# Performance work log

Hardware: AMD Instinct MI355X
Metric: run time of the kernel (lower is better)

Reference implementation:

```python
import jax, jax.numpy as jnp
import numpy as np

ROPE_BASE = 10000.0

def _rms_norm(x):
    eps = jnp.asarray(jnp.finfo(x.dtype).eps, x.dtype)
    return x * jax.lax.rsqrt(jnp.mean(x * x, axis=-1, keepdims=True) + eps)

def _rope(x):
    # x: [B, S, H, hd]; rotate-halves variant: y1 = x1*cos + x2*sin, y2 = -x1*sin + x2*cos
    S, hd = x.shape[1], x.shape[3]
    d = hd // 2
    inv_freq = 1.0 / (ROPE_BASE ** (jnp.arange(0, hd, 2, dtype=jnp.float32) / hd))  # [d]
    t = jnp.arange(S, dtype=jnp.float32)
    freqs = jnp.outer(t, inv_freq)                       # [S, d]
    cos = jnp.cos(freqs)[None, :, None, :].astype(x.dtype)
    sin = jnp.sin(freqs)[None, :, None, :].astype(x.dtype)
    x1, x2 = x[..., :d], x[..., d:]
    return jnp.concatenate([x1 * cos + x2 * sin, -x1 * sin + x2 * cos], axis=-1)

def setup_inputs() -> dict:
    key = jax.random.key(0)
    ks = jax.random.split(key, 7)
    B, S, D = 1, 2048, 1024
    std = 0.02
    return {
        "x": jax.random.normal(ks[0], (B, S, D), jnp.float32),
        "v1": jax.random.normal(ks[1], (B, S, D), jnp.float32),
        "Wq": jax.random.normal(ks[2], (D, D), jnp.float32) * std,
        "Wk": jax.random.normal(ks[3], (D, D), jnp.float32) * std,
        "Wv": jax.random.normal(ks[4], (D, D), jnp.float32) * std,
        "Wout": jax.random.normal(ks[5], (D, D), jnp.float32) * std,
        "lambdas": jnp.float32(0.5),
        "n_heads": 16,
    }

def reference(x, v1, Wq, Wk, Wv, Wout, lambdas, n_heads):
    B, S, D = x.shape
    H = n_heads
    hd = D // H
    # QKV projections (CastedLinear, no bias)
    q = (x @ Wq.T).reshape(B, S, H, hd)
    k = (x @ Wk.T).reshape(B, S, H, hd)
    v = (x @ Wv.T).reshape(B, S, H, hd)
    # value residual mix with first-layer values v1
    v = (1.0 - lambdas) * v + lambdas * v1.reshape(B, S, H, hd)
    # per-head RMS norm (no learned scale) then RoPE
    q, k = _rms_norm(q), _rms_norm(k)
    q, k = _rope(q), _rope(k)
    # causal attention (flex_attention default: softmax, scale 1/sqrt(hd))
    scale = 1.0 / jnp.sqrt(jnp.asarray(hd, x.dtype))
    scores = jnp.einsum('bqhd,bkhd->bhqk', q, k) * scale        # [B,H,S,S]
    causal = jnp.tril(jnp.ones((S, S), dtype=bool))
    scores = jnp.where(causal[None, None], scores, jnp.asarray(-jnp.inf, scores.dtype))
    p = jax.nn.softmax(scores, axis=-1)
    y = jnp.einsum('bhqk,bkhd->bqhd', p, v).reshape(B, S, D)
    y = y @ Wout.T
    return (y, v1)
```

## Files before the change

kernel.cpp:

```cpp
#include <hip/hip_runtime.h>
#include <hip/hip_bf16.h>

#define S_LEN 2048
#define D_DIM 1024
#define NH    16
#define NEG_BIG (-1.0e30f)

#define EPI_NORMROPE   1
#define EPI_VMIX_T     2
#define EPI_F32        3
#define EPI_NORMROPE_Q 4
#define EPI_F32A       5

typedef __attribute__((ext_vector_type(8))) short bf16x8;
typedef __attribute__((ext_vector_type(4))) float f32x4;
typedef const __attribute__((address_space(1))) unsigned char gu8_t;
typedef __attribute__((address_space(3))) unsigned char lu8_t;

__device__ __forceinline__ float bf2f(unsigned short h) {
    union { unsigned int u; float f; } v; v.u = ((unsigned int)h) << 16; return v.f;
}
__device__ __forceinline__ unsigned short f2b(float f) {
    union { float f; unsigned int u; } v; v.f = f;
    unsigned int u = v.u;
    return (unsigned short)((u + 0x7FFFu + ((u >> 16) & 1u)) >> 16);
}
__device__ __forceinline__ unsigned short f2b_trunc(float f) {
    union { float f; unsigned int u; } v; v.f = f;
    return (unsigned short)(v.u >> 16);
}

__global__ __launch_bounds__(256)
void to_bf16(const float* __restrict__ x,  const float* __restrict__ wq,
             const float* __restrict__ wk, const float* __restrict__ wv,
             const float* __restrict__ wo, const float* __restrict__ v1,
             unsigned short* __restrict__ xb,  unsigned short* __restrict__ wqb,
             unsigned short* __restrict__ wkb, unsigned short* __restrict__ wvb,
             unsigned short* __restrict__ wob, float* __restrict__ v1dst)
{
    const int z = blockIdx.y;
    int i8 = blockIdx.x * 256 + threadIdx.x;
    if (z == 5) {
        const float* sp = v1 + (size_t)i8 * 8;
        float4 lo = *(const float4*)sp, hi = *(const float4*)(sp + 4);
        float* dp = v1dst + (size_t)i8 * 8;
        *(float4*)dp = lo; *(float4*)(dp + 4) = hi;
        return;
    }
    const float* s; unsigned short* d; int n;
    switch (z) {
        case 0: s = x;  d = xb;  n = S_LEN * D_DIM; break;
        case 1: s = wq; d = wqb; n = D_DIM * D_DIM; break;
        case 2: s = wk; d = wkb; n = D_DIM * D_DIM; break;
        case 3: s = wv; d = wvb; n = D_DIM * D_DIM; break;
        default: s = wo; d = wob; n = D_DIM * D_DIM; break;
    }
    if (i8 * 8 >= n) return;
    const float* sp = s + (size_t)i8 * 8;
    float4 lo = *(const float4*)sp, hi = *(const float4*)(sp + 4);
    uint4 p;
    p.x = f2b(lo.x) | ((unsigned)f2b(lo.y) << 16);
    p.y = f2b(lo.z) | ((unsigned)f2b(lo.w) << 16);
    p.z = f2b(hi.x) | ((unsigned)f2b(hi.y) << 16);
    p.w = f2b(hi.z) | ((unsigned)f2b(hi.w) << 16);
    *(uint4*)(d + (size_t)i8 * 8) = p;
}

__global__ __launch_bounds__(256, 3)
void gemm64(const unsigned short* __restrict__ A,
            const unsigned short* __restrict__ B0, const unsigned short* __restrict__ B1,
            const unsigned short* __restrict__ B2,
            void* __restrict__ C0, void* __restrict__ C1, void* __restrict__ C2,
            const float* __restrict__ vmix, const float* __restrict__ lam,
            int epiPack)
{
    const int which = blockIdx.z;
    const unsigned short* Bp = (which == 0) ? B0 : ((which == 1) ? B1 : B2);
    void* C = (which == 0) ? C0 : ((which == 1) ? C1 : C2);
    const int epi = (epiPack >> (8 * which)) & 0xff;
    const int tn = blockIdx.x * 128;
    const int tm = blockIdx.y * 64;

    __shared__ unsigned short Asl[64 * 32];
    __shared__ unsigned short Bsl[128 * 32];

    const int t    = threadIdx.x;
    const int lane = t & 63;
    const int wave = t >> 6;
    const int wm   = (wave >> 1) * 32;
    const int wn   = (wave & 1) * 64;
    const int lrow = lane & 15;
    const int quad = lane >> 4;
    const int srow = t >> 2;
    const int scol = (t & 3) * 8;

    f32x4 acc[2][4];
    #pragma unroll
    for (int i = 0; i < 2; ++i)
        #pragma unroll
        for (int j = 0; j < 4; ++j) {
            f32x4 z = {0.f, 0.f, 0.f, 0.f};
            acc[i][j] = z;
        }

    for (int k0 = 0; k0 < D_DIM; k0 += 32) {
        __builtin_amdgcn_global_load_lds(
            (gu8_t*)(A + (size_t)(tm + srow) * D_DIM + k0 + scol),
            (lu8_t*)&Asl[t * 8], 16, 0, 0);
        __builtin_amdgcn_global_load_lds(
            (gu8_t*)(Bp + (size_t)(tn + srow) * D_DIM + k0 + scol),
            (lu8_t*)&Bsl[t * 8], 16, 0, 0);
        __builtin_amdgcn_global_load_lds(
            (gu8_t*)(Bp + (size_t)(tn + 64 + srow) * D_DIM + k0 + scol),
            (lu8_t*)&Bsl[2048 + t * 8], 16, 0, 0);
        __syncthreads();
        bf16x8 af[2], bfr[4];
        #pragma unroll
        for (int i = 0; i < 2; ++i)
            af[i] = *(const bf16x8*)(&Asl[(wm + i * 16 + lrow) * 32 + quad * 8]);
        #pragma unroll
        for (int j = 0; j < 4; ++j)
            bfr[j] = *(const bf16x8*)(&Bsl[(wn + j * 16 + lrow) * 32 + quad * 8]);
        #pragma unroll
        for (int i = 0; i < 2; ++i)
            #pragma unroll
            for (int j = 0; j < 4; ++j)
                acc[i][j] = __builtin_amdgcn_mfma_f32_16x16x32_bf16(af[i], bfr[j], acc[i][j], 0, 0, 0);
        __syncthreads();
    }

    if (epi == EPI_NORMROPE || epi == EPI_NORMROPE_Q) {
        const float post = (epi == EPI_NORMROPE_Q) ? 0.18033688011112042f : 1.0f;
        #pragma unroll
        for (int i = 0; i < 2; ++i) {
            #pragma unroll
            for (int r = 0; r < 4; ++r) {
                int row = tm + wm + i * 16 + quad * 4 + r;
                float v0 = acc[i][0][r], v1 = acc[i][1][r];
                float v2 = acc[i][2][r], v3 = acc[i][3][r];
                float ss = v0 * v0 + v1 * v1 + v2 * v2 + v3 * v3;
                ss += __shfl_xor(ss, 1); ss += __shfl_xor(ss, 2);
                ss += __shfl_xor(ss, 4); ss += __shfl_xor(ss, 8);
                float rms = rsqrtf(ss * (1.f / 64.f) + 1.1920929e-7f) * post;
                v0 *= rms; v1 *= rms; v2 *= rms; v3 *= rms;
                float fs = (float)row;
                float a0 = fs * exp2f(-0.41524101186092030f * (float)lrow);
                float a1 = fs * exp2f(-0.41524101186092030f * (float)(16 + lrow));
                float s0, c0, s1, c1;
                __sincosf(a0, &s0, &c0);
                __sincosf(a1, &s1, &c1);
                unsigned short* Cb = (unsigned short*)C;
                size_t base = (size_t)row * D_DIM + tn + wn + lrow;
                Cb[base]      = f2b(v0 * c0 + v2 * s0);
                Cb[base + 16] = f2b(v1 * c1 + v3 * s1);
                Cb[base + 32] = f2b(-v0 * s0 + v2 * c0);
                Cb[base + 48] = f2b(-v1 * s1 + v3 * c1);
            }
        }
    } else if (epi == EPI_VMIX_T) {
        float lamf = *lam;
        #pragma unroll
        for (int i = 0; i < 2; ++i) {
            int cm0 = tm + wm + i * 16 + quad * 4;
            #pragma unroll
            for (int j = 0; j < 4; ++j) {
                int cn = tn + wn + j * 16 + lrow;
                ushort4 pk;
                float vals[4];
                #pragma unroll
                for (int r = 0; r < 4; ++r) {
                    size_t idx = (size_t)(cm0 + r) * D_DIM + cn;
                    vals[r] = (1.f - lamf) * acc[i][j][r] + lamf * vmix[idx];
                }
                pk.x = f2b(vals[0]); pk.y = f2b(vals[1]);
                pk.z = f2b(vals[2]); pk.w = f2b(vals[3]);
                *(ushort4*)((unsigned short*)C + (size_t)cn * S_LEN + cm0) = pk;
            }
        }
    } else {
        #pragma unroll
        for (int i = 0; i < 2; ++i) {
            int cm0 = tm + wm + i * 16 + quad * 4;
            #pragma unroll
            for (int j = 0; j < 4; ++j) {
                int cn = tn + wn + j * 16 + lrow;
                #pragma unroll
                for (int r = 0; r < 4; ++r)
                    ((float*)C)[(size_t)(cm0 + r) * D_DIM + cn] = acc[i][j][r];
            }
        }
    }
}

__global__ __launch_bounds__(256, 3)
void gemm_bt(const unsigned short* __restrict__ A,
             const unsigned short* __restrict__ B0,
             void* __restrict__ C0,
             const float* __restrict__ lam,
             int epi, int splitK)
{
    const int which = blockIdx.z;
    const unsigned short* Bp = B0;
    void* C = C0;
    int kLo = 0, kHi = D_DIM;
    if (splitK) { kLo = which * (D_DIM / 2); kHi = kLo + D_DIM / 2; }
    const int tn = blockIdx.x * 128;
    const int tm = blockIdx.y * 128;

    __shared__ unsigned short Asl[128 * 32];
    __shared__ unsigned short Bsl[128 * 32];

    const int t    = threadIdx.x;
    const int lane = t & 63;
    const int wave = t >> 6;
    const int wm   = (wave >> 1) * 64;
    const int wn   = (wave & 1) * 64;
    const int lrow = lane & 15;
    const int quad = lane >> 4;
    const int srow = lane >> 2;
    const int scol = (lane & 3) * 8;

    f32x4 acc[4][4];
    #pragma unroll
    for (int i = 0; i < 4; ++i)
        #pragma unroll
        for (int j = 0; j < 4; ++j) {
            f32x4 z = {0.f, 0.f, 0.f, 0.f};
            acc[i][j] = z;
        }

    for (int k0 = kLo; k0 < kHi; k0 += 32) {
        #pragma unroll
        for (int rep = 0; rep < 2; ++rep) {
            int grp = wave * 2 + rep;
            int row = grp * 16 + srow;
            __builtin_amdgcn_global_load_lds(
                (gu8_t*)(A + (size_t)(tm + row) * D_DIM + k0 + scol),
                (lu8_t*)&Asl[grp * 512], 16, 0, 0);
            __builtin_amdgcn_global_load_lds(
                (gu8_t*)(Bp + (size_t)(tn + row) * D_DIM + k0 + scol),
                (lu8_t*)&Bsl[grp * 512], 16, 0, 0);
        }
        __syncthreads();
        bf16x8 af[4], bfr[4];
        #pragma unroll
        for (int i = 0; i < 4; ++i)
            af[i] = *(const bf16x8*)(&Asl[(wm + i * 16 + lrow) * 32 + quad * 8]);
        #pragma unroll
        for (int j = 0; j < 4; ++j)
            bfr[j] = *(const bf16x8*)(&Bsl[(wn + j * 16 + lrow) * 32 + quad * 8]);
        #pragma unroll
        for (int i = 0; i < 4; ++i)
            #pragma unroll
            for (int j = 0; j < 4; ++j)
                acc[i][j] = __builtin_amdgcn_mfma_f32_16x16x32_bf16(af[i], bfr[j], acc[i][j], 0, 0, 0);
        __syncthreads();
    }

    if (epi == EPI_F32A) {
        #pragma unroll
        for (int i = 0; i < 4; ++i) {
            int cm0 = tm + wm + i * 16 + quad * 4;
            #pragma unroll
            for (int j = 0; j < 4; ++j) {
                int cn = tn + wn + j * 16 + lrow;
                #pragma unroll
                for (int r = 0; r < 4; ++r)
                    atomicAdd(&((float*)C)[(size_t)(cm0 + r) * D_DIM + cn], acc[i][j][r]);
            }
        }
    } else {
        #pragma unroll
        for (int i = 0; i < 4; ++i) {
            int cm0 = tm + wm + i * 16 + quad * 4;
            #pragma unroll
            for (int j = 0; j < 4; ++j) {
                int cn = tn + wn + j * 16 + lrow;
                #pragma unroll
                for (int r = 0; r < 4; ++r)
                    ((float*)C)[(size_t)(cm0 + r) * D_DIM + cn] = acc[i][j][r];
            }
        }
    }
}

__global__ __launch_bounds__(256, 4)
void attn_mfma(const unsigned short* Qb,
               const unsigned short* __restrict__ Kb,
               const unsigned short* __restrict__ Vtg,
               float* __restrict__ Opart, float* __restrict__ Lpart)
{
    const int bx = blockIdx.x;
    int qt, c;
    if (bx < 32)      { qt = 31 - (bx >> 2);            c = bx & 3;  }
    else if (bx < 56) { int i = bx - 32; qt = 23 - i/3; c = i % 3;   }
    else if (bx < 72) { int i = bx - 56; qt = 15 - (i>>1); c = i & 1;}
    else              { qt = 7 - (bx - 72);             c = 0;       }
    const int jlo = c * 8;
    const int jhi = min(jlo + 7, qt);
    const int h  = blockIdx.y;
    const int t  = threadIdx.x;
    const int w  = t >> 6;
    const int l  = t & 63;
    const int l15  = l & 15;
    const int quad = l >> 4;
    const int hco  = h * 64;
    const int slot = (qt * 4 + c) * NH + h;

    __shared__ unsigned short Ks[2][64][72];
    __shared__ unsigned short Vt[2][64][72];

    const unsigned short* qrow = Qb + (size_t)(qt * 64 + w * 16 + l15) * D_DIM + hco;
    bf16x8 qf0 = *(const bf16x8*)(qrow + quad * 8);
    bf16x8 qf1 = *(const bf16x8*)(qrow + 32 + quad * 8);

    f32x4 oac[4];
    #pragma unroll
    for (int nt = 0; nt < 4; ++nt) { f32x4 z = {0.f,0.f,0.f,0.f}; oac[nt] = z; }
    float lsum = 0.f;

    const int rr = t >> 2;
    const int dc = (t & 3) * 16;

    const unsigned short* kbase = Kb  + (size_t)rr * D_DIM + hco + dc;
    const unsigned short* vbase = Vtg + (size_t)(hco + rr) * S_LEN + dc;

    uint4 ka0, ka1, va0, va1;
    {
        const unsigned short* kp = kbase + (size_t)jlo * 64 * D_DIM;
        const unsigned short* vp = vbase + (size_t)jlo * 64;
        ka0 = *(const uint4*)kp;  ka1 = *(const uint4*)(kp + 8);
        va0 = *(const uint4*)vp;  va1 = *(const uint4*)(vp + 8);
    }

    const int q_g = qt * 64 + w * 16 + l15;
    const float C2 = -11.541560327111707f;

    for (int j = jlo; j <= jhi; ++j) {
        const int buf = (j - jlo) & 1;
        *(uint4*)&Ks[buf][rr][dc]     = ka0;
        *(uint4*)&Ks[buf][rr][dc + 8] = ka1;
        *(uint4*)&Vt[buf][rr][dc]     = va0;
        *(uint4*)&Vt[buf][rr][dc + 8] = va1;
        __syncthreads();
        if (j < jhi) {
            const unsigned short* kp = kbase + (size_t)(j + 1) * 64 * D_DIM;
            const unsigned short* vp = vbase + (size_t)(j + 1) * 64;
            ka0 = *(const uint4*)kp;  ka1 = *(const uint4*)(kp + 8);
            va0 = *(const uint4*)vp;  va1 = *(const uint4*)(vp + 8);
        }

        f32x4 sac[4];
        __builtin_amdgcn_s_setprio(1);
        #pragma unroll
        for (int nt = 0; nt < 4; ++nt) {
            f32x4 z = {0.f,0.f,0.f,0.f};
            bf16x8 kf0 = *(const bf16x8*)&Ks[buf][nt * 16 + l15][quad * 8];
            z = __builtin_amdgcn_mfma_f32_16x16x32_bf16(kf0, qf0, z, 0, 0, 0);
            bf16x8 kf1 = *(const bf16x8*)&Ks[buf][nt * 16 + l15][32 + quad * 8];
            z = __builtin_amdgcn_mfma_f32_16x16x32_bf16(kf1, qf1, z, 0, 0, 0);
            sac[nt] = z;
        }
        __builtin_amdgcn_s_setprio(0);

        unsigned short (*Psw)[72] = (unsigned short (*)[72])&Ks[buf ^ 1][w * 16];

        if (j < qt) {
            #pragma unroll
            for (int nt = 0; nt < 4; ++nt) {
                float pe0 = exp2f(sac[nt][0] + C2);
                float pe1 = exp2f(sac[nt][1] + C2);
                float pe2 = exp2f(sac[nt][2] + C2);
                float pe3 = exp2f(sac[nt][3] + C2);
                lsum += (pe0 + pe1) + (pe2 + pe3);
                ushort4 pk;
                pk.x = f2b_trunc(pe0); pk.y = f2b_trunc(pe1);
                pk.z = f2b_trunc(pe2); pk.w = f2b_trunc(pe3);
                *(ushort4*)&Psw[l15][nt * 16 + quad * 4] = pk;
            }
        } else {
            #pragma unroll
            for (int nt = 0; nt < 4; ++nt) {
                int key0 = j * 64 + nt * 16 + quad * 4;
                float pe[4];
                #pragma unroll
                for (int r = 0; r < 4; ++r) {
                    float s = sac[nt][r] + C2;
                    if (key0 + r > q_g) s = NEG_BIG;
                    pe[r] = exp2f(s);
                    lsum += pe[r];
                }
                ushort4 pk;
                pk.x = f2b_trunc(pe[0]); pk.y = f2b_trunc(pe[1]);
                pk.z = f2b_trunc(pe[2]); pk.w = f2b_trunc(pe[3]);
                *(ushort4*)&Psw[l15][nt * 16 + quad * 4] = pk;
            }
        }

        bf16x8 pf0 = *(const bf16x8*)&Psw[l15][quad * 8];
        bf16x8 pf1 = *(const bf16x8*)&Psw[l15][32 + quad * 8];
        __builtin_amdgcn_s_setprio(1);
        #pragma unroll
        for (int nt = 0; nt < 4; ++nt) {
            bf16x8 vf0 = *(const bf16x8*)&Vt[buf][nt * 16 + l15][quad * 8];
            oac[nt] = __builtin_amdgcn_mfma_f32_16x16x32_bf16(pf0, vf0, oac[nt], 0, 0, 0);
            bf16x8 vf1 = *(const bf16x8*)&Vt[buf][nt * 16 + l15][32 + quad * 8];
            oac[nt] = __builtin_amdgcn_mfma_f32_16x16x32_bf16(pf1, vf1, oac[nt], 0, 0, 0);
        }
        __builtin_amdgcn_s_setprio(0);
        __syncthreads();
    }

    float lr = lsum;
    lr += __shfl_xor(lr, 16);
    lr += __shfl_xor(lr, 32);
    if (l < 16)
        Lpart[(size_t)slot * 64 + w * 16 + l15] = lr;
    float* Op = Opart + (size_t)slot * 4096;
    #pragma unroll
    for (int nt = 0; nt < 4; ++nt)
        #pragma unroll
        for (int r = 0; r < 4; ++r)
            Op[(size_t)(w * 16 + quad * 4 + r) * 64 + nt * 16 + l15] = oac[nt][r];
}

__global__ __launch_bounds__(256)
void attn_combine(const float* __restrict__ Opart, const float* __restrict__ Lpart,
                  unsigned short* __restrict__ Ob, float* __restrict__ yzero)
{
    const int qt  = blockIdx.x;
    const int h   = blockIdx.y;
    const int t   = threadIdx.x;
    const int row = t >> 2;
    const int c0  = (t & 3) * 16;
    float acc[16];
    #pragma unroll
    for (int i = 0; i < 16; ++i) acc[i] = 0.f;
    float lsum = 0.f;
    for (int c = 0; c < 4; ++c) {
        if (c * 8 > qt) break;
        const size_t slot = (size_t)((qt * 4 + c) * NH + h);
        const float* Op = Opart + slot * 4096 + (size_t)row * 64 + c0;
        #pragma unroll
        for (int g = 0; g < 4; ++g) {
            float4 a = *(const float4*)(Op + g * 4);
            acc[g * 4 + 0] += a.x; acc[g * 4 + 1] += a.y;
            acc[g * 4 + 2] += a.z; acc[g * 4 + 3] += a.w;
        }
        lsum += Lpart[slot * 64 + row];
    }
    const float inv = 1.f / lsum;
    unsigned int pk[8];
    #pragma unroll
    for (int i = 0; i < 8; ++i)
        pk[i] = f2b(acc[2 * i] * inv) | ((unsigned)f2b(acc[2 * i + 1] * inv) << 16);
    unsigned short* dst = Ob + (size_t)(qt * 64 + row) * D_DIM + h * 64 + c0;
    *(uint4*)dst       = make_uint4(pk[0], pk[1], pk[2], pk[3]);
    *(uint4*)(dst + 8) = make_uint4(pk[4], pk[5], pk[6], pk[7]);

    const int flat = (h * 32 + qt) * 256 + t;
    float4 z4 = {0.f, 0.f, 0.f, 0.f};
    float4* yz = (float4*)(yzero + (size_t)flat * 16);
    yz[0] = z4; yz[1] = z4; yz[2] = z4; yz[3] = z4;
}

extern "C" void kernel_launch(void* const* d_in, const int* in_sizes, int n_in,
                              void* d_out, int out_size, void* d_ws, size_t ws_size,
                              hipStream_t stream)
{
    const float* x    = (const float*)d_in[0];
    const float* v1   = (const float*)d_in[1];
    const float* Wq   = (const float*)d_in[2];
    const float* Wk   = (const float*)d_in[3];
    const float* Wv   = (const float*)d_in[4];
    const float* Wout = (const float*)d_in[5];
    const float* lam  = (const float*)d_in[6];
    float* out = (float*)d_out;

    const size_t SD = (size_t)S_LEN * D_DIM;
    const size_t DD = (size_t)D_DIM * D_DIM;
    unsigned short* Qb  = (unsigned short*)d_ws;
    unsigned short* Kb  = Qb + SD;
    unsigned short* Vtg = Kb + SD;
    unsigned short* Ab  = Qb;
    float* Opart = (float*)(Vtg + SD);
    float* Lpart = Opart + (size_t)2048 * 4096;
    unsigned short* xb    = (unsigned short*)((char*)d_ws + (46u << 20));
    unsigned short* Woutb = (unsigned short*)((char*)d_ws + (50u << 20));

    unsigned short* Wqb   = (unsigned short*)d_out;
    unsigned short* Wkb   = Wqb + DD;
    unsigned short* Wvb   = Wkb + DD;

    to_bf16<<<dim3(1024, 6), 256, 0, stream>>>(
        x, Wq, Wk, Wv, Wout, v1, xb, Wqb, Wkb, Wvb, Woutb, out + SD);

    gemm64<<<dim3(D_DIM / 128, S_LEN / 64, 3), 256, 0, stream>>>(
        xb, Wqb, Wkb, Wvb, Qb, Kb, Vtg, v1, lam,
        EPI_NORMROPE_Q | (EPI_NORMROPE << 8) | (EPI_VMIX_T << 16));

    attn_mfma<<<dim3(80, NH), 256, 0, stream>>>(Qb, Kb, Vtg, Opart, Lpart);
    attn_combine<<<dim3(S_LEN / 64, NH), 256, 0, stream>>>(Opart, Lpart, Ab, out);

    gemm_bt<<<dim3(D_DIM / 128, S_LEN / 128, 2), 256, 0, stream>>>(
        Ab, Woutb, d_out, lam, EPI_F32A, 1);
}
```

Measured before the change: 173.4 us.

## Use 128-row query tiles in attention and replace split-K output GEMM

```diff
diff --git a/kernel.cpp b/kernel.cpp
--- a/kernel.cpp
+++ b/kernel.cpp
@@ -10,7 +10,6 @@
 #define EPI_VMIX_T     2
 #define EPI_F32        3
 #define EPI_NORMROPE_Q 4
-#define EPI_F32A       5
 
 typedef __attribute__((ext_vector_type(8))) short bf16x8;
 typedef __attribute__((ext_vector_type(4))) float f32x4;
@@ -192,98 +191,6 @@
     }
 }
 
-__global__ __launch_bounds__(256, 3)
-void gemm_bt(const unsigned short* __restrict__ A,
-             const unsigned short* __restrict__ B0,
-             void* __restrict__ C0,
-             const float* __restrict__ lam,
-             int epi, int splitK)
-{
-    const int which = blockIdx.z;
-    const unsigned short* Bp = B0;
-    void* C = C0;
-    int kLo = 0, kHi = D_DIM;
-    if (splitK) { kLo = which * (D_DIM / 2); kHi = kLo + D_DIM / 2; }
-    const int tn = blockIdx.x * 128;
-    const int tm = blockIdx.y * 128;
-
-    __shared__ unsigned short Asl[128 * 32];
-    __shared__ unsigned short Bsl[128 * 32];
-
-    const int t    = threadIdx.x;
-    const int lane = t & 63;
-    const int wave = t >> 6;
-    const int wm   = (wave >> 1) * 64;
-    const int wn   = (wave & 1) * 64;
-    const int lrow = lane & 15;
-    const int quad = lane >> 4;
-    const int srow = lane >> 2;
-    const int scol = (lane & 3) * 8;
-
-    f32x4 acc[4][4];
-    #pragma unroll
-    for (int i = 0; i < 4; ++i)
-        #pragma unroll
-        for (int j = 0; j < 4; ++j) {
-            f32x4 z = {0.f, 0.f, 0.f, 0.f};
-            acc[i][j] = z;
-        }
-
-    for (int k0 = kLo; k0 < kHi; k0 += 32) {
-        #pragma unroll
-        for (int rep = 0; rep < 2; ++rep) {
-            int grp = wave * 2 + rep;
-            int row = grp * 16 + srow;
-            __builtin_amdgcn_global_load_lds(
-                (gu8_t*)(A + (size_t)(tm + row) * D_DIM + k0 + scol),
-                (lu8_t*)&Asl[grp * 512], 16, 0, 0);
-            __builtin_amdgcn_global_load_lds(
-                (gu8_t*)(Bp + (size_t)(tn + row) * D_DIM + k0 + scol),
-                (lu8_t*)&Bsl[grp * 512], 16, 0, 0);
-        }
-        __syncthreads();
-        bf16x8 af[4], bfr[4];
-        #pragma unroll
-        for (int i = 0; i < 4; ++i)
-            af[i] = *(const bf16x8*)(&Asl[(wm + i * 16 + lrow) * 32 + quad * 8]);
-        #pragma unroll
-        for (int j = 0; j < 4; ++j)
-            bfr[j] = *(const bf16x8*)(&Bsl[(wn + j * 16 + lrow) * 32 + quad * 8]);
-        #pragma unroll
-        for (int i = 0; i < 4; ++i)
-            #pragma unroll
-            for (int j = 0; j < 4; ++j)
-                acc[i][j] = __builtin_amdgcn_mfma_f32_16x16x32_bf16(af[i], bfr[j], acc[i][j], 0, 0, 0);
-        __syncthreads();
-    }
-
-    if (epi == EPI_F32A) {
-        #pragma unroll
-        for (int i = 0; i < 4; ++i) {
-            int cm0 = tm + wm + i * 16 + quad * 4;
-            #pragma unroll
-            for (int j = 0; j < 4; ++j) {
-                int cn = tn + wn + j * 16 + lrow;
-                #pragma unroll
-                for (int r = 0; r < 4; ++r)
-                    atomicAdd(&((float*)C)[(size_t)(cm0 + r) * D_DIM + cn], acc[i][j][r]);
-            }
-        }
-    } else {
-        #pragma unroll
-        for (int i = 0; i < 4; ++i) {
-            int cm0 = tm + wm + i * 16 + quad * 4;
-            #pragma unroll
-            for (int j = 0; j < 4; ++j) {
-                int cn = tn + wn + j * 16 + lrow;
-                #pragma unroll
-                for (int r = 0; r < 4; ++r)
-                    ((float*)C)[(size_t)(cm0 + r) * D_DIM + cn] = acc[i][j][r];
-            }
-        }
-    }
-}
-
 __global__ __launch_bounds__(256, 4)
 void attn_mfma(const unsigned short* Qb,
                const unsigned short* __restrict__ Kb,
@@ -291,13 +198,19 @@
                float* __restrict__ Opart, float* __restrict__ Lpart)
 {
     const int bx = blockIdx.x;
-    int qt, c;
-    if (bx < 32)      { qt = 31 - (bx >> 2);            c = bx & 3;  }
-    else if (bx < 56) { int i = bx - 32; qt = 23 - i/3; c = i % 3;   }
-    else if (bx < 72) { int i = bx - 56; qt = 15 - (i>>1); c = i & 1;}
-    else              { qt = 7 - (bx - 72);             c = 0;       }
-    const int jlo = c * 8;
-    const int jhi = min(jlo + 7, qt);
+    int qb = 0, c = 0;
+    {
+        int accum = 0;
+        #pragma unroll
+        for (int q = 15; q >= 0; --q) {
+            int n = (2 * q + 9) >> 3;
+            if (bx >= accum && bx < accum + n) { qb = q; c = bx - accum; }
+            accum += n;
+        }
+    }
+    const int jmax = 2 * qb + 1;
+    const int jlo  = c * 8;
+    const int jhi  = min(jlo + 7, jmax);
     const int h  = blockIdx.y;
     const int t  = threadIdx.x;
     const int w  = t >> 6;
@@ -305,19 +218,26 @@
     const int l15  = l & 15;
     const int quad = l >> 4;
     const int hco  = h * 64;
-    const int slot = (qt * 4 + c) * NH + h;
+    const int slot = (qb * 4 + c) * NH + h;
 
     __shared__ unsigned short Ks[2][64][72];
     __shared__ unsigned short Vt[2][64][72];
 
-    const unsigned short* qrow = Qb + (size_t)(qt * 64 + w * 16 + l15) * D_DIM + hco;
-    bf16x8 qf0 = *(const bf16x8*)(qrow + quad * 8);
-    bf16x8 qf1 = *(const bf16x8*)(qrow + 32 + quad * 8);
-
-    f32x4 oac[4];
-    #pragma unroll
-    for (int nt = 0; nt < 4; ++nt) { f32x4 z = {0.f,0.f,0.f,0.f}; oac[nt] = z; }
-    float lsum = 0.f;
+    bf16x8 qf[2][2];
+    #pragma unroll
+    for (int g = 0; g < 2; ++g) {
+        const unsigned short* qrow =
+            Qb + (size_t)(qb * 128 + w * 32 + g * 16 + l15) * D_DIM + hco;
+        qf[g][0] = *(const bf16x8*)(qrow + quad * 8);
+        qf[g][1] = *(const bf16x8*)(qrow + 32 + quad * 8);
+    }
+
+    f32x4 oac[2][4];
+    #pragma unroll
+    for (int g = 0; g < 2; ++g)
+        #pragma unroll
+        for (int nt = 0; nt < 4; ++nt) { f32x4 z = {0.f,0.f,0.f,0.f}; oac[g][nt] = z; }
+    float lsum0 = 0.f, lsum1 = 0.f;
 
     const int rr = t >> 2;
     const int dc = (t & 3) * 16;
@@ -333,7 +253,6 @@
         va0 = *(const uint4*)vp;  va1 = *(const uint4*)(vp + 8);
     }
 
-    const int q_g = qt * 64 + w * 16 + l15;
     const float C2 = -11.541560327111707f;
 
     for (int j = jlo; j <= jhi; ++j) {
@@ -350,118 +269,130 @@
             va0 = *(const uint4*)vp;  va1 = *(const uint4*)(vp + 8);
         }
 
-        f32x4 sac[4];
-        __builtin_amdgcn_s_setprio(1);
-        #pragma unroll
-        for (int nt = 0; nt < 4; ++nt) {
-            f32x4 z = {0.f,0.f,0.f,0.f};
-            bf16x8 kf0 = *(const bf16x8*)&Ks[buf][nt * 16 + l15][quad * 8];
-            z = __builtin_amdgcn_mfma_f32_16x16x32_bf16(kf0, qf0, z, 0, 0, 0);
-            bf16x8 kf1 = *(const bf16x8*)&Ks[buf][nt * 16 + l15][32 + quad * 8];
-            z = __builtin_amdgcn_mfma_f32_16x16x32_bf16(kf1, qf1, z, 0, 0, 0);
-            sac[nt] = z;
-        }
-        __builtin_amdgcn_s_setprio(0);
-
-        unsigned short (*Psw)[72] = (unsigned short (*)[72])&Ks[buf ^ 1][w * 16];
-
-        if (j < qt) {
+        unsigned short (*stale)[72] = (w < 2)
+            ? (unsigned short (*)[72])&Ks[buf ^ 1][w * 32]
+            : (unsigned short (*)[72])&Vt[buf ^ 1][(w - 2) * 32];
+        const bool bulk = (j < 2 * qb);
+
+        #pragma unroll
+        for (int g = 0; g < 2; ++g) {
+            f32x4 sac[4];
+            __builtin_amdgcn_s_setprio(1);
             #pragma unroll
             for (int nt = 0; nt < 4; ++nt) {
-                float pe0 = exp2f(sac[nt][0] + C2);
-                float pe1 = exp2f(sac[nt][1] + C2);
-                float pe2 = exp2f(sac[nt][2] + C2);
-                float pe3 = exp2f(sac[nt][3] + C2);
-                lsum += (pe0 + pe1) + (pe2 + pe3);
-                ushort4 pk;
-                pk.x = f2b_trunc(pe0); pk.y = f2b_trunc(pe1);
-                pk.z = f2b_trunc(pe2); pk.w = f2b_trunc(pe3);
-                *(ushort4*)&Psw[l15][nt * 16 + quad * 4] = pk;
-            }
-        } else {
+                f32x4 z = {0.f,0.f,0.f,0.f};
+                bf16x8 kf0 = *(const bf16x8*)&Ks[buf][nt * 16 + l15][quad * 8];
+                z = __builtin_amdgcn_mfma_f32_16x16x32_bf16(kf0, qf[g][0], z, 0, 0, 0);
+                bf16x8 kf1 = *(const bf16x8*)&Ks[buf][nt * 16 + l15][32 + quad * 8];
+                z = __builtin_amdgcn_mfma_f32_16x16x32_bf16(kf1, qf[g][1], z, 0, 0, 0);
+                sac[nt] = z;
+            }
+            __builtin_amdgcn_s_setprio(0);
+
+            unsigned short (*Psw)[72] = (unsigned short (*)[72])&stale[g * 16];
+            float lg = 0.f;
+            if (bulk) {
+                #pragma unroll
+                for (int nt = 0; nt < 4; ++nt) {
+                    float pe0 = exp2f(sac[nt][0] + C2);
+                    float pe1 = exp2f(sac[nt][1] + C2);
+                    float pe2 = exp2f(sac[nt][2] + C2);
+                    float pe3 = exp2f(sac[nt][3] + C2);
+                    lg += (pe0 + pe1) + (pe2 + pe3);
+                    ushort4 pk;
+                    pk.x = f2b_trunc(pe0); pk.y = f2b_trunc(pe1);
+                    pk.z = f2b_trunc(pe2); pk.w = f2b_trunc(pe3);
+                    *(ushort4*)&Psw[l15][nt * 16 + quad * 4] = pk;
+                }
+            } else {
+                const int q_g = qb * 128 + w * 32 + g * 16 + l15;
+                #pragma unroll
+                for (int nt = 0; nt < 4; ++nt) {
+                    int key0 = j * 64 + nt * 16 + quad * 4;
+                    float pe[4];
+                    #pragma unroll
+                    for (int r = 0; r < 4; ++r) {
+                        float s = sac[nt][r] + C2;
+                        if (key0 + r > q_g) s = NEG_BIG;
+                        pe[r] = exp2f(s);
+                        lg += pe[r];
+                    }
+                    ushort4 pk;
+                    pk.x = f2b_trunc(pe[0]); pk.y = f2b_trunc(pe[1]);
+                    pk.z = f2b_trunc(pe[2]); pk.w = f2b_trunc(pe[3]);
+                    *(ushort4*)&Psw[l15][nt * 16 + quad * 4] = pk;
+                }
+            }
+            if (g == 0) lsum0 += lg; else lsum1 += lg;
+
+            bf16x8 pf0 = *(const bf16x8*)&Psw[l15][quad * 8];
+            bf16x8 pf1 = *(const bf16x8*)&Psw[l15][32 + quad * 8];
+            __builtin_amdgcn_s_setprio(1);
             #pragma unroll
             for (int nt = 0; nt < 4; ++nt) {
-                int key0 = j * 64 + nt * 16 + quad * 4;
-                float pe[4];
-                #pragma unroll
-                for (int r = 0; r < 4; ++r) {
-                    float s = sac[nt][r] + C2;
-                    if (key0 + r > q_g) s = NEG_BIG;
-                    pe[r] = exp2f(s);
-                    lsum += pe[r];
-                }
-                ushort4 pk;
-                pk.x = f2b_trunc(pe[0]); pk.y = f2b_trunc(pe[1]);
-                pk.z = f2b_trunc(pe[2]); pk.w = f2b_trunc(pe[3]);
-                *(ushort4*)&Psw[l15][nt * 16 + quad * 4] = pk;
-            }
-        }
-
-        bf16x8 pf0 = *(const bf16x8*)&Psw[l15][quad * 8];
-        bf16x8 pf1 = *(const bf16x8*)&Psw[l15][32 + quad * 8];
-        __builtin_amdgcn_s_setprio(1);
-        #pragma unroll
-        for (int nt = 0; nt < 4; ++nt) {
-            bf16x8 vf0 = *(const bf16x8*)&Vt[buf][nt * 16 + l15][quad * 8];
-            oac[nt] = __builtin_amdgcn_mfma_f32_16x16x32_bf16(pf0, vf0, oac[nt], 0, 0, 0);
-            bf16x8 vf1 = *(const bf16x8*)&Vt[buf][nt * 16 + l15][32 + quad * 8];
-            oac[nt] = __builtin_amdgcn_mfma_f32_16x16x32_bf16(pf1, vf1, oac[nt], 0, 0, 0);
-        }
-        __builtin_amdgcn_s_setprio(0);
+                bf16x8 vf0 = *(const bf16x8*)&Vt[buf][nt * 16 + l15][quad * 8];
+                oac[g][nt] = __builtin_amdgcn_mfma_f32_16x16x32_bf16(pf0, vf0, oac[g][nt], 0, 0, 0);
+                bf16x8 vf1 = *(const bf16x8*)&Vt[buf][nt * 16 + l15][32 + quad * 8];
+                oac[g][nt] = __builtin_amdgcn_mfma_f32_16x16x32_bf16(pf1, vf1, oac[g][nt], 0, 0, 0);
+            }
+            __builtin_amdgcn_s_setprio(0);
+        }
         __syncthreads();
     }
 
-    float lr = lsum;
-    lr += __shfl_xor(lr, 16);
-    lr += __shfl_xor(lr, 32);
-    if (l < 16)
-        Lpart[(size_t)slot * 64 + w * 16 + l15] = lr;
-    float* Op = Opart + (size_t)slot * 4096;
-    #pragma unroll
-    for (int nt = 0; nt < 4; ++nt)
-        #pragma unroll
-        for (int r = 0; r < 4; ++r)
-            Op[(size_t)(w * 16 + quad * 4 + r) * 64 + nt * 16 + l15] = oac[nt][r];
+    #pragma unroll
+    for (int g = 0; g < 2; ++g) {
+        float lr = (g == 0) ? lsum0 : lsum1;
+        lr += __shfl_xor(lr, 16);
+        lr += __shfl_xor(lr, 32);
+        if (l < 16)
+            Lpart[(size_t)slot * 128 + w * 32 + g * 16 + l15] = lr;
+    }
+    float* Op = Opart + (size_t)slot * 8192;
+    #pragma unroll
+    for (int g = 0; g < 2; ++g)
+        #pragma unroll
+        for (int nt = 0; nt < 4; ++nt)
+            #pragma unroll
+            for (int r = 0; r < 4; ++r)
+                Op[(size_t)(w * 32 + g * 16 + quad * 4 + r) * 64 + nt * 16 + l15] = oac[g][nt][r];
 }
 
 __global__ __launch_bounds__(256)
 void attn_combine(const float* __restrict__ Opart, const float* __restrict__ Lpart,
-                  unsigned short* __restrict__ Ob, float* __restrict__ yzero)
+                  unsigned short* __restrict__ Ob)
 {
-    const int qt  = blockIdx.x;
+    const int qb  = blockIdx.x;
     const int h   = blockIdx.y;
     const int t   = threadIdx.x;
-    const int row = t >> 2;
-    const int c0  = (t & 3) * 16;
-    float acc[16];
-    #pragma unroll
-    for (int i = 0; i < 16; ++i) acc[i] = 0.f;
+    const int row = t >> 1;
+    const int c0  = (t & 1) * 32;
+    const int nchunks = (2 * qb + 9) >> 3;
+    float acc[32];
+    #pragma unroll
+    for (int i = 0; i < 32; ++i) acc[i] = 0.f;
     float lsum = 0.f;
-    for (int c = 0; c < 4; ++c) {
-        if (c * 8 > qt) break;
-        const size_t slot = (size_t)((qt * 4 + c) * NH + h);
-        const float* Op = Opart + slot * 4096 + (size_t)row * 64 + c0;
-        #pragma unroll
-        for (int g = 0; g < 4; ++g) {
+    for (int c = 0; c < nchunks; ++c) {
+        const size_t slot = (size_t)((qb * 4 + c) * NH + h);
+        const float* Op = Opart + slot * 8192 + (size_t)row * 64 + c0;
+        #pragma unroll
+        for (int g = 0; g < 8; ++g) {
             float4 a = *(const float4*)(Op + g * 4);
             acc[g * 4 + 0] += a.x; acc[g * 4 + 1] += a.y;
             acc[g * 4 + 2] += a.z; acc[g * 4 + 3] += a.w;
         }
-        lsum += Lpart[slot * 64 + row];
+        lsum += Lpart[slot * 128 + row];
     }
     const float inv = 1.f / lsum;
-    unsigned int pk[8];
-    #pragma unroll
-    for (int i = 0; i < 8; ++i)
+    unsigned int pk[16];
+    #pragma unroll
+    for (int i = 0; i < 16; ++i)
         pk[i] = f2b(acc[2 * i] * inv) | ((unsigned)f2b(acc[2 * i + 1] * inv) << 16);
-    unsigned short* dst = Ob + (size_t)(qt * 64 + row) * D_DIM + h * 64 + c0;
-    *(uint4*)dst       = make_uint4(pk[0], pk[1], pk[2], pk[3]);
-    *(uint4*)(dst + 8) = make_uint4(pk[4], pk[5], pk[6], pk[7]);
-
-    const int flat = (h * 32 + qt) * 256 + t;
-    float4 z4 = {0.f, 0.f, 0.f, 0.f};
-    float4* yz = (float4*)(yzero + (size_t)flat * 16);
-    yz[0] = z4; yz[1] = z4; yz[2] = z4; yz[3] = z4;
+    unsigned short* dst = Ob + (size_t)(qb * 128 + row) * D_DIM + h * 64 + c0;
+    *(uint4*)dst        = make_uint4(pk[0],  pk[1],  pk[2],  pk[3]);
+    *(uint4*)(dst + 8)  = make_uint4(pk[4],  pk[5],  pk[6],  pk[7]);
+    *(uint4*)(dst + 16) = make_uint4(pk[8],  pk[9],  pk[10], pk[11]);
+    *(uint4*)(dst + 24) = make_uint4(pk[12], pk[13], pk[14], pk[15]);
 }
 
 extern "C" void kernel_launch(void* const* d_in, const int* in_sizes, int n_in,
@@ -484,7 +415,7 @@
     unsigned short* Vtg = Kb + SD;
     unsigned short* Ab  = Qb;
     float* Opart = (float*)(Vtg + SD);
-    float* Lpart = Opart + (size_t)2048 * 4096;
+    float* Lpart = Opart + (size_t)1024 * 8192;
     unsigned short* xb    = (unsigned short*)((char*)d_ws + (46u << 20));
     unsigned short* Woutb = (unsigned short*)((char*)d_ws + (50u << 20));
 
@@ -499,9 +430,9 @@
         xb, Wqb, Wkb, Wvb, Qb, Kb, Vtg, v1, lam,
         EPI_NORMROPE_Q | (EPI_NORMROPE << 8) | (EPI_VMIX_T << 16));
 
-    attn_mfma<<<dim3(80, NH), 256, 0, stream>>>(Qb, Kb, Vtg, Opart, Lpart);
-    attn_combine<<<dim3(S_LEN / 64, NH), 256, 0, stream>>>(Opart, Lpart, Ab, out);
-
-    gemm_bt<<<dim3(D_DIM / 128, S_LEN / 128, 2), 256, 0, stream>>>(
-        Ab, Woutb, d_out, lam, EPI_F32A, 1);
-}
+    attn_mfma<<<dim3(40, NH), 256, 0, stream>>>(Qb, Kb, Vtg, Opart, Lpart);
+    attn_combine<<<dim3(S_LEN / 128, NH), 256, 0, stream>>>(Opart, Lpart, Ab);
+
+    gemm64<<<dim3(D_DIM / 128, S_LEN / 64, 1), 256, 0, stream>>>(
+        Ab, Woutb, Woutb, Woutb, d_out, d_out, d_out, nullptr, lam, EPI_F32);
+}
```

Measured after the change: 170.3 us. About the same (-1.8%).
